# Performance work log

Hardware: AMD Instinct MI355X
Metric: run time of the kernel (lower is better)

The kernel has to match this reference:

```python
import jax, jax.numpy as jnp
import numpy as np

B, T, C = 2, 2048, 1024
H, HS = 16, 64
THETA = 10000.0


def _rope_tables(seq_len, dim, dtype):
    inv_freq = 1.0 / (THETA ** (jnp.arange(0, dim, 2, dtype=jnp.float32) / dim))
    t = jnp.arange(seq_len, dtype=jnp.float32)
    freqs = t[:, None] * inv_freq[None, :]          # [T, dim/2]
    emb = jnp.concatenate([freqs, freqs], axis=-1)  # [T, dim]
    return jnp.cos(emb).astype(dtype), jnp.sin(emb).astype(dtype)


def _rotate_half(x):
    x1, x2 = jnp.split(x, 2, axis=-1)
    return jnp.concatenate([-x2, x1], axis=-1)


def setup_inputs() -> dict:
    key = jax.random.key(0)
    ks = jax.random.split(key, 9)
    s = 0.02
    return {
        "q_x": jax.random.normal(ks[0], (B, T, C), dtype=jnp.float32),
        "wq": jax.random.normal(ks[1], (C, H * HS), dtype=jnp.float32) * s,
        "bq": jnp.zeros((H * HS,), dtype=jnp.float32),
        "wk": jax.random.normal(ks[2], (C, H * HS), dtype=jnp.float32) * s,
        "bk": jnp.zeros((H * HS,), dtype=jnp.float32),
        "wv": jax.random.normal(ks[3], (C, H * HS), dtype=jnp.float32) * s,
        "bv": jnp.zeros((H * HS,), dtype=jnp.float32),
        "wc": jax.random.normal(ks[4], (H * HS, C), dtype=jnp.float32) * s,
        "bc": jnp.zeros((C,), dtype=jnp.float32),
    }


def reference(q_x, wq, bq, wk, bk, wv, bv, wc, bc):
    b, t, _ = q_x.shape
    # Q/K/V projections -> [B, H, T, HS]
    q = (q_x @ wq + bq).reshape(b, t, H, HS).transpose(0, 2, 1, 3)
    k = (q_x @ wk + bk).reshape(b, t, H, HS).transpose(0, 2, 1, 3)
    v = (q_x @ wv + bv).reshape(b, t, H, HS).transpose(0, 2, 1, 3)
    # RoPE (concat-half rotation)
    cos, sin = _rope_tables(t, HS, q.dtype)  # [T, HS]
    q = q * cos + _rotate_half(q) * sin
    k = k * cos + _rotate_half(k) * sin
    # Naive causal attention
    scale = 1.0 / np.sqrt(HS)
    att = jnp.einsum("bhqd,bhkd->bhqk", q, k) * scale
    mask = jnp.tril(jnp.ones((t, t), dtype=bool))
    att = jnp.where(mask, att, -jnp.inf)
    att = jax.nn.softmax(att, axis=-1)
    y = jnp.einsum("bhqk,bhkd->bhqd", att, v)
    y = y.transpose(0, 2, 1, 3).reshape(b, t, H * HS)
    return y @ wc + bc
```

## Files before the change

### kernel.cpp

```cpp
#include <hip/hip_runtime.h>

#define B_  2
#define T_  2048
#define C_  1024
#define H_  16
#define HS_ 64
#define M_  4096
#define N_  1024
#define K_  1024

typedef float floatx4 __attribute__((ext_vector_type(4)));
typedef short bf16x8  __attribute__((ext_vector_type(8)));

__device__ __forceinline__ float bf2f(unsigned short u) {
    return __uint_as_float(((unsigned int)u) << 16);
}
__device__ __forceinline__ unsigned short f2bf(float f) {
    unsigned int u = __float_as_uint(f);
    return (unsigned short)((u + 0x7fffu + ((u >> 16) & 1u)) >> 16);
}
__device__ __forceinline__ unsigned int pack2(float a, float b) {
    return (unsigned int)f2bf(a) | ((unsigned int)f2bf(b) << 16);
}
__device__ __forceinline__ unsigned int pack2t(float a, float b) {
    return __builtin_amdgcn_perm(__float_as_uint(b), __float_as_uint(a), 0x07060302u);
}
__device__ __forceinline__ void async16(const unsigned short* g, unsigned short* l) {
    __builtin_amdgcn_global_load_lds(
        (const __attribute__((address_space(1))) unsigned int*)g,
        (__attribute__((address_space(3))) unsigned int*)l, 16, 0, 0);
}

__global__ __launch_bounds__(256) void prep_kernel(
    const float* __restrict__ x,
    const float* __restrict__ w0, const float* __restrict__ w1,
    const float* __restrict__ w2, const float* __restrict__ w3,
    unsigned short* __restrict__ xb, unsigned short* __restrict__ wTall)
{
    __shared__ float tile[64][65];
    const int bid = blockIdx.x;
    const int t = threadIdx.x;
    if (bid < 4096) {
        const size_t i = ((size_t)bid * 256 + t) * 4;
        const float4 v = *(const float4*)(x + i);
        ushort4 st;
        st.x = f2bf(v.x); st.y = f2bf(v.y); st.z = f2bf(v.z); st.w = f2bf(v.w);
        *(ushort4*)(xb + i) = st;
        return;
    }
    const int zb = bid - 4096;
    const int z = zb >> 8, rem = zb & 255;
    const float* w = (z == 0) ? w0 : (z == 1) ? w1 : (z == 2) ? w2 : w3;
    unsigned short* wT = wTall + ((size_t)z << 20);
    const int n0 = (rem & 15) * 64, k0 = (rem >> 4) * 64;

    const int r = t >> 2, cq = (t & 3) * 16;
    const float4* src = (const float4*)(w + (size_t)(k0 + r) * N_ + n0 + cq);
    const float4 v0 = src[0], v1 = src[1], v2 = src[2], v3 = src[3];
    tile[r][cq+0]=v0.x; tile[r][cq+1]=v0.y; tile[r][cq+2]=v0.z; tile[r][cq+3]=v0.w;
    tile[r][cq+4]=v1.x; tile[r][cq+5]=v1.y; tile[r][cq+6]=v1.z; tile[r][cq+7]=v1.w;
    tile[r][cq+8]=v2.x; tile[r][cq+9]=v2.y; tile[r][cq+10]=v2.z; tile[r][cq+11]=v2.w;
    tile[r][cq+12]=v3.x; tile[r][cq+13]=v3.y; tile[r][cq+14]=v3.z; tile[r][cq+15]=v3.w;
    __syncthreads();

    const int rn = t >> 2, ck = (t & 3) * 16;
    unsigned int o[8];
#pragma unroll
    for (int ii = 0; ii < 8; ii++)
        o[ii] = pack2(tile[ck + 2*ii][rn], tile[ck + 2*ii + 1][rn]);
    unsigned short* dst = wT + (size_t)(n0 + rn) * K_ + k0 + ck;
    *(uint4*)dst       = make_uint4(o[0], o[1], o[2], o[3]);
    *(uint4*)(dst + 8) = make_uint4(o[4], o[5], o[6], o[7]);
}

__global__ __launch_bounds__(512, 2) void qkv_gemm(
    const unsigned short* __restrict__ xb, const unsigned short* __restrict__ wT,
    const float* __restrict__ bq, const float* __restrict__ bk,
    const float* __restrict__ bv,
    unsigned short* __restrict__ qb, unsigned short* __restrict__ kb,
    unsigned short* __restrict__ vb)
{
    __shared__ unsigned short lds[65536];

    const int tid  = threadIdx.x;
    const int lane = tid & 63;
    const int wave = tid >> 6;

    const int bid = blockIdx.x;
    const int swz = (bid & 7) * 24 + (bid >> 3);
    const int nb  = swz % 12;
    const int mb  = swz / 12;
    const int m0  = mb * 256;
    const int n0g = nb * 256;

    const int wm = wave >> 2, wn = wave & 3;
    const int fr = lane & 15, quad = lane >> 4;

    const int r_s = tid >> 2;
    const int c_s = (tid & 3) ^ ((tid >> 3) & 3);
    const unsigned short* aS0 = xb + (size_t)(m0 + r_s) * 1024 + c_s * 8;
    const unsigned short* aS1 = aS0 + (size_t)128 * 1024;
    const unsigned short* bS0 = wT + (size_t)(n0g + r_s) * 1024 + c_s * 8;
    const unsigned short* bS1 = bS0 + (size_t)128 * 1024;
    unsigned short* ldw = &lds[wave * 512];

    auto stage = [&](int buf, int region, const unsigned short* s0,
                     const unsigned short* s1) {
        unsigned short* d = ldw + buf * 32768 + region * 8192;
        async16(s0, d);
        async16(s1, d + 4096);
    };

    int oA[8], oB[4];
#pragma unroll
    for (int i = 0; i < 8; i++) {
        const int r = wm * 128 + i * 16 + fr;
        oA[i] = r * 32 + ((quad ^ ((r >> 1) & 3)) << 3);
    }
#pragma unroll
    for (int j = 0; j < 4; j++) {
        const int r = wn * 64 + j * 16 + fr;
        oB[j] = r * 32 + ((quad ^ ((r >> 1) & 3)) << 3);
    }

    floatx4 acc[8][4];
#pragma unroll
    for (int i = 0; i < 8; i++)
#pragma unroll
        for (int j = 0; j < 4; j++) acc[i][j] = (floatx4){0.f, 0.f, 0.f, 0.f};

    stage(0, 0, aS0,      aS1);
    stage(0, 2, bS0,      bS1);
    stage(0, 1, aS0 + 32, aS1 + 32);
    stage(0, 3, bS0 + 32, bS1 + 32);
    stage(1, 0, aS0 + 64, aS1 + 64);
    stage(1, 2, bS0 + 64, bS1 + 64);
    asm volatile("s_waitcnt vmcnt(8)" ::: "memory");
    __builtin_amdgcn_s_barrier();
    __builtin_amdgcn_sched_barrier(0);

    bf16x8 af[4], bfr[4];
#pragma unroll 2
    for (int t = 0; t < 16; ++t) {
        const int cur = t & 1, nxt = cur ^ 1;
        const unsigned short* A0 = &lds[cur * 32768];
        const unsigned short* A1 = A0 + 8192;
        const unsigned short* B0 = A0 + 16384;
        const unsigned short* B1 = A0 + 24576;
        const int k1 = (t + 1) * 64, k2 = (t + 2) * 64;

#pragma unroll
        for (int i = 0; i < 4; i++) af[i]  = *(const bf16x8*)&A0[oA[i]];
#pragma unroll
        for (int j = 0; j < 4; j++) bfr[j] = *(const bf16x8*)&B0[oB[j]];
        if (t + 1 < 16) stage(nxt, 1, aS0 + k1 + 32, aS1 + k1 + 32);
        __builtin_amdgcn_s_barrier();
        asm volatile("s_waitcnt lgkmcnt(0)" ::: "memory");
        __builtin_amdgcn_s_setprio(1);
#pragma unroll
        for (int i = 0; i < 4; i++)
#pragma unroll
            for (int j = 0; j < 4; j++)
                acc[i][j] = __builtin_amdgcn_mfma_f32_16x16x32_bf16(
                    af[i], bfr[j], acc[i][j], 0, 0, 0);
        __builtin_amdgcn_s_setprio(0);
        __builtin_amdgcn_s_barrier();
        __builtin_amdgcn_sched_barrier(0);

#pragma unroll
        for (int i = 0; i < 4; i++) af[i] = *(const bf16x8*)&A0[oA[4 + i]];
        if (t + 1 < 16) stage(nxt, 3, bS0 + k1 + 32, bS1 + k1 + 32);
        asm volatile("s_waitcnt vmcnt(8)" ::: "memory");
        __builtin_amdgcn_s_barrier();
        asm volatile("s_waitcnt lgkmcnt(0)" ::: "memory");
        __builtin_amdgcn_s_setprio(1);
#pragma unroll
        for (int i = 0; i < 4; i++)
#pragma unroll
            for (int j = 0; j < 4; j++)
                acc[4 + i][j] = __builtin_amdgcn_mfma_f32_16x16x32_bf16(
                    af[i], bfr[j], acc[4 + i][j], 0, 0, 0);
        __builtin_amdgcn_s_setprio(0);
        __builtin_amdgcn_s_barrier();
        __builtin_amdgcn_sched_barrier(0);

#pragma unroll
        for (int i = 0; i < 4; i++) af[i]  = *(const bf16x8*)&A1[oA[i]];
#pragma unroll
        for (int j = 0; j < 4; j++) bfr[j] = *(const bf16x8*)&B1[oB[j]];
        if (t + 2 < 16) stage(cur, 0, aS0 + k2, aS1 + k2);
        __builtin_amdgcn_s_barrier();
        asm volatile("s_waitcnt lgkmcnt(0)" ::: "memory");
        __builtin_amdgcn_s_setprio(1);
#pragma unroll
        for (int i = 0; i < 4; i++)
#pragma unroll
            for (int j = 0; j < 4; j++)
                acc[i][j] = __builtin_amdgcn_mfma_f32_16x16x32_bf16(
                    af[i], bfr[j], acc[i][j], 0, 0, 0);
        __builtin_amdgcn_s_setprio(0);
        __builtin_amdgcn_s_barrier();
        __builtin_amdgcn_sched_barrier(0);

#pragma unroll
        for (int i = 0; i < 4; i++) af[i] = *(const bf16x8*)&A1[oA[4 + i]];
        if (t + 2 < 16) stage(cur, 2, bS0 + k2, bS1 + k2);
        asm volatile("s_waitcnt vmcnt(8)" ::: "memory");
        __builtin_amdgcn_s_barrier();
        asm volatile("s_waitcnt lgkmcnt(0)" ::: "memory");
        __builtin_amdgcn_s_setprio(1);
#pragma unroll
        for (int i = 0; i < 4; i++)
#pragma unroll
            for (int j = 0; j < 4; j++)
                acc[4 + i][j] = __builtin_amdgcn_mfma_f32_16x16x32_bf16(
                    af[i], bfr[j], acc[4 + i][j], 0, 0, 0);
        __builtin_amdgcn_s_setprio(0);
        __builtin_amdgcn_s_barrier();
        __builtin_amdgcn_sched_barrier(0);
    }

    const int p = nb >> 2;
    const int colbase = (nb & 3) * 256 + wn * 64;
    const int h = colbase >> 6;
    const int rb = quad * 4;
    const float* bias = (p == 0) ? bq : (p == 1) ? bk : bv;

    if (p == 2) {
#pragma unroll
        for (int j = 0; j < 4; j++) {
            const int d = j * 16 + fr;
            const float bz = bias[colbase + d];
#pragma unroll
            for (int i = 0; i < 8; i++) {
                const int row0 = m0 + wm * 128 + i * 16 + rb;
                const int bb = row0 >> 11, tt = row0 & 2047;
                ushort4 st;
                st.x = f2bf(acc[i][j][0] + bz);
                st.y = f2bf(acc[i][j][1] + bz);
                st.z = f2bf(acc[i][j][2] + bz);
                st.w = f2bf(acc[i][j][3] + bz);
                *(ushort4*)&vb[((size_t)(bb * H_ + h) * HS_ + d) * T_ + tt] = st;
            }
        }
    } else {
        unsigned short* out = (p == 0) ? qb : kb;
        const float qsc = (p == 0) ? 0.18033688011111772f : 1.0f;
        const float bz0 = bias[colbase + fr];
        const float bz1 = bias[colbase + 16 + fr];
        const float bz2 = bias[colbase + 32 + fr];
        const float bz3 = bias[colbase + 48 + fr];
        const float nl = -0.41524101186279297f;
        const float if0 = exp2f((float)fr * nl);
        const float if1 = exp2f((float)(fr + 16) * nl);
#pragma unroll
        for (int i = 0; i < 8; i++) {
#pragma unroll
            for (int pr = 0; pr < 4; pr++) {
                const int row = m0 + wm * 128 + i * 16 + rb + pr;
                const int bb = row >> 11, tt = row & 2047;
                float s0, c0, s1, c1;
                __sincosf((float)tt * if0, &s0, &c0);
                __sincosf((float)tt * if1, &s1, &c1);
                const float v0 = acc[i][0][pr] + bz0;
                const float v1 = acc[i][1][pr] + bz1;
                const float v2 = acc[i][2][pr] + bz2;
                const float v3 = acc[i][3][pr] + bz3;
                unsigned short* ob = out + ((size_t)(bb * H_ + h) * T_ + tt) * HS_ + fr;
                ob[0]  = f2bf((v0 * c0 - v2 * s0) * qsc);
                ob[16] = f2bf((v1 * c1 - v3 * s1) * qsc);
                ob[32] = f2bf((v2 * c0 + v0 * s0) * qsc);
                ob[48] = f2bf((v3 * c1 + v1 * s1) * qsc);
            }
        }
    }
}

__global__ __launch_bounds__(256) void attn_kernel(
    const unsigned short* __restrict__ qb, const unsigned short* __restrict__ kb,
    const unsigned short* __restrict__ vt, unsigned short* __restrict__ yb,
    unsigned short* __restrict__ Opart, float* __restrict__ Mpart)
{
    __shared__ unsigned short Ks[2][64 * 64];
    __shared__ unsigned short Vs[2][64 * 64];
    __shared__ unsigned short Ps[4][16 * 64];

    const int bh = blockIdx.x;
    const int b = bh >> 4, h = bh & 15;
    const int s = 47 - (int)blockIdx.y;
    int qt, ktlo, kthi, half;
    bool split;
    if (s < 16) { qt = s; ktlo = 0; kthi = qt; half = 0; split = false; }
    else {
        const int idx = s - 16;
        qt = 16 + (idx >> 1); half = idx & 1;
        const int nf = (qt + 2) >> 1;
        ktlo = half ? nf : 0;
        kthi = half ? qt : nf - 1;
        split = true;
    }
    const int r0 = qt * 64;
    const int tid  = threadIdx.x;
    const int lane = tid & 63;
    const int wave = tid >> 6;
    const int l4   = lane & 15;
    const int quad = lane >> 4;

    const int qrow_g = r0 + wave * 16 + l4;

    bf16x8 qf[2];
    {
        const unsigned short* qp = qb + ((size_t)bh * T_ + qrow_g) * HS_ + quad * 8;
        qf[0] = *(const bf16x8*)(qp);
        qf[1] = *(const bf16x8*)(qp + 32);
    }

    floatx4 o[4];
#pragma unroll
    for (int g = 0; g < 4; g++) o[g] = (floatx4){0.f, 0.f, 0.f, 0.f};
    float m = -1e30f, l = 0.f;

    const int srow = tid >> 2;
    const int sc16 = (tid & 3) * 16;
    const int ssw  = (srow & 7) * 8;
    const int psw  = (l4 & 7) * 8;

    const unsigned short* kp = kb + ((size_t)bh * T_ + srow) * HS_ + sc16;
    const unsigned short* vp = vt + ((size_t)(bh * 64 + srow)) * T_ + sc16;

    uint4 rk0 = *(const uint4*)(kp + (size_t)ktlo * 64 * HS_);
    uint4 rk1 = *(const uint4*)(kp + (size_t)ktlo * 64 * HS_ + 8);
    uint4 rv0 = *(const uint4*)(vp + ktlo * 64);
    uint4 rv1 = *(const uint4*)(vp + ktlo * 64 + 8);
    *(uint4*)&Ks[0][srow * 64 + ( sc16      ^ ssw)] = rk0;
    *(uint4*)&Ks[0][srow * 64 + ((sc16 + 8) ^ ssw)] = rk1;
    *(uint4*)&Vs[0][srow * 64 + ( sc16      ^ ssw)] = rv0;
    *(uint4*)&Vs[0][srow * 64 + ((sc16 + 8) ^ ssw)] = rv1;

    for (int kt = ktlo; kt <= kthi; kt++) {
        const int cur = (kt - ktlo) & 1;
        if (kt < kthi) {
            const unsigned short* kpn = kp + (size_t)(kt + 1) * (64 * HS_);
            const unsigned short* vpn = vp + (kt + 1) * 64;
            rk0 = *(const uint4*)kpn;
            rk1 = *(const uint4*)(kpn + 8);
            rv0 = *(const uint4*)vpn;
            rv1 = *(const uint4*)(vpn + 8);
        }
        __syncthreads();

        floatx4 sf[4];
#pragma unroll
        for (int mg = 0; mg < 4; mg++) {
            const int key = mg * 16 + l4;
            const int ksw = (key & 7) * 8;
            const bf16x8 a0 = *(const bf16x8*)&Ks[cur][key * 64 + ( (quad * 8)       ^ ksw)];
            const bf16x8 a1 = *(const bf16x8*)&Ks[cur][key * 64 + (((quad * 8) + 32) ^ ksw)];
            floatx4 z = (floatx4){0.f, 0.f, 0.f, 0.f};
            z = __builtin_amdgcn_mfma_f32_16x16x32_bf16(a0, qf[0], z, 0, 0, 0);
            z = __builtin_amdgcn_mfma_f32_16x16x32_bf16(a1, qf[1], z, 0, 0, 0);
            sf[mg] = z;
        }

        if (kt == qt) {
#pragma unroll
            for (int mg = 0; mg < 4; mg++)
#pragma unroll
                for (int r = 0; r < 4; r++)
                    if (kt * 64 + 16 * mg + quad * 4 + r > qrow_g)
                        sf[mg][r] = -1e30f;
        }

        float tm = sf[0][0];
#pragma unroll
        for (int mg = 0; mg < 4; mg++)
#pragma unroll
            for (int r = 0; r < 4; r++) tm = fmaxf(tm, sf[mg][r]);
        tm = fmaxf(tm, __shfl_xor(tm, 16));
        tm = fmaxf(tm, __shfl_xor(tm, 32));
        const float mnew  = fmaxf(m, tm);
        const float alpha = __builtin_amdgcn_exp2f(m - mnew);

        float p[4][4];
        float ps = 0.f;
#pragma unroll
        for (int mg = 0; mg < 4; mg++)
#pragma unroll
            for (int r = 0; r < 4; r++) {
                p[mg][r] = __builtin_amdgcn_exp2f(sf[mg][r] - mnew);
                ps += p[mg][r];
            }
        ps += __shfl_xor(ps, 16);
        ps += __shfl_xor(ps, 32);
        l = l * alpha + ps;
        m = mnew;
#pragma unroll
        for (int g = 0; g < 4; g++) o[g] = o[g] * alpha;

#pragma unroll
        for (int mg = 0; mg < 4; mg++) {
            const int kb4 = 16 * mg + quad * 4;
            const int off = ((kb4 & ~7) ^ psw) | (kb4 & 7);
            uint2 w;
            w.x = pack2t(p[mg][0], p[mg][1]);
            w.y = pack2t(p[mg][2], p[mg][3]);
            *(uint2*)&Ps[wave][l4 * 64 + off] = w;
        }

        const bf16x8 pf0 = *(const bf16x8*)&Ps[wave][l4 * 64 + ( (quad * 8)       ^ psw)];
        const bf16x8 pf1 = *(const bf16x8*)&Ps[wave][l4 * 64 + (((quad * 8) + 32) ^ psw)];
#pragma unroll
        for (int g = 0; g < 4; g++) {
            const int vd  = g * 16 + l4;
            const int vsw = (vd & 7) * 8;
            const bf16x8 va0 = *(const bf16x8*)&Vs[cur][vd * 64 + ( (quad * 8)       ^ vsw)];
            const bf16x8 va1 = *(const bf16x8*)&Vs[cur][vd * 64 + (((quad * 8) + 32) ^ vsw)];
            o[g] = __builtin_amdgcn_mfma_f32_16x16x32_bf16(va0, pf0, o[g], 0, 0, 0);
            o[g] = __builtin_amdgcn_mfma_f32_16x16x32_bf16(va1, pf1, o[g], 0, 0, 0);
        }

        if (kt < kthi) {
            const int nxt = cur ^ 1;
            *(uint4*)&Ks[nxt][srow * 64 + ( sc16      ^ ssw)] = rk0;
            *(uint4*)&Ks[nxt][srow * 64 + ((sc16 + 8) ^ ssw)] = rk1;
            *(uint4*)&Vs[nxt][srow * 64 + ( sc16      ^ ssw)] = rv0;
            *(uint4*)&Vs[nxt][srow * 64 + ((sc16 + 8) ^ ssw)] = rv1;
        }
    }

    if (!split) {
        const float invl = 1.f / l;
        unsigned short* yrow = yb + ((size_t)(b * T_ + qrow_g) * H_ + h) * HS_;
#pragma unroll
        for (int g = 0; g < 4; g++) {
            ushort4 st;
            st.x = f2bf(o[g][0] * invl);
            st.y = f2bf(o[g][1] * invl);
            st.z = f2bf(o[g][2] * invl);
            st.w = f2bf(o[g][3] * invl);
            *(ushort4*)&yrow[16 * g + quad * 4] = st;
        }
    } else {
        const int u  = (bh * 16 + (qt - 16)) * 2 + half;
        const int rl = wave * 16 + l4;
        unsigned short* Op = Opart + (size_t)u * 4096 + rl * 64;
#pragma unroll
        for (int g = 0; g < 4; g++) {
            ushort4 st;
            st.x = f2bf(o[g][0]);
            st.y = f2bf(o[g][1]);
            st.z = f2bf(o[g][2]);
            st.w = f2bf(o[g][3]);
            *(ushort4*)&Op[16 * g + quad * 4] = st;
        }
        if (quad == 0) {
            float* ml = Mpart + (size_t)u * 128;
            ml[rl]      = m;
            ml[64 + rl] = l;
        }
    }
}

__global__ __launch_bounds__(256) void attn_combine(
    const unsigned short* __restrict__ Opart, const float* __restrict__ Mpart,
    unsigned short* __restrict__ yb)
{
    const int u  = blockIdx.x;
    const int bh = u >> 4, qt = 16 + (u & 15);
    const int b = bh >> 4, h = bh & 15;
    const int t = threadIdx.x;
    const int r = t >> 2, c = (t & 3) * 16;

    const float* ml1 = Mpart + (size_t)(u * 2) * 128;
    const float* ml2 = ml1 + 128;
    const float m1 = ml1[r], l1 = ml1[64 + r];
    const float m2 = ml2[r], l2 = ml2[64 + r];
    const float M  = fmaxf(m1, m2);
    const float w1 = __builtin_amdgcn_exp2f(m1 - M);
    const float w2 = __builtin_amdgcn_exp2f(m2 - M);
    const float inv = 1.f / (l1 * w1 + l2 * w2);
    const float a1 = w1 * inv, a2 = w2 * inv;

    const unsigned short* O1 = Opart + (size_t)(u * 2)     * 4096 + r * 64 + c;
    const unsigned short* O2 = Opart + (size_t)(u * 2 + 1) * 4096 + r * 64 + c;
    unsigned short* yrow = yb + ((size_t)(b * T_ + qt * 64 + r) * H_ + h) * HS_ + c;

#pragma unroll
    for (int j = 0; j < 2; j++) {
        const uint4 u1 = *(const uint4*)(O1 + 8 * j);
        const uint4 u2 = *(const uint4*)(O2 + 8 * j);
        const unsigned int a[4] = {u1.x, u1.y, u1.z, u1.w};
        const unsigned int d[4] = {u2.x, u2.y, u2.z, u2.w};
        unsigned int ov[4];
#pragma unroll
        for (int q = 0; q < 4; q++) {
            const float y0 = bf2f((unsigned short)(a[q] & 0xffff)) * a1
                           + bf2f((unsigned short)(d[q] & 0xffff)) * a2;
            const float y1 = bf2f((unsigned short)(a[q] >> 16)) * a1
                           + bf2f((unsigned short)(d[q] >> 16)) * a2;
            ov[q] = pack2(y0, y1);
        }
        *(uint4*)(yrow + 8 * j) = make_uint4(ov[0], ov[1], ov[2], ov[3]);
    }
}

__global__ __launch_bounds__(256) void out_gemm(
    const unsigned short* __restrict__ A, const unsigned short* __restrict__ wcT,
    const float* __restrict__ bias, float* __restrict__ out)
{
    __shared__ unsigned short As[2 * 64 * 32];
    __shared__ unsigned short Bs[2 * 128 * 32];

    const int tid  = threadIdx.x;
    const int lane = tid & 63;
    const int wave = tid >> 6;
    const int n0 = blockIdx.x * 128;
    const int m0 = blockIdx.y * 64;

    const int lrow = lane >> 2, lch = (lane & 3) * 8;
    const unsigned short* ag  = A   + (size_t)(m0 + wave * 16 + lrow) * K_ + lch;
    const unsigned short* bg0 = wcT + (size_t)(n0 + wave * 32 + lrow) * K_ + lch;
    const unsigned short* bg1 = bg0 + (size_t)16 * K_;
    unsigned short* lA0  = &As[(wave * 16) * 32];
    unsigned short* lA1  = lA0 + 2048;
    unsigned short* lB00 = &Bs[(wave * 32) * 32];
    unsigned short* lB01 = &Bs[(wave * 32 + 16) * 32];
    unsigned short* lB10 = lB00 + 4096;
    unsigned short* lB11 = lB01 + 4096;

    const int fr = lane & 15;
    const int fk = (lane >> 4) * 8;
    const int wr2 = wave >> 1, wc2 = wave & 1;

    floatx4 acc[2][4];
#pragma unroll
    for (int i = 0; i < 2; i++)
#pragma unroll
        for (int j = 0; j < 4; j++) acc[i][j] = (floatx4){0.f, 0.f, 0.f, 0.f};

    for (int k0 = 0; k0 < K_; k0 += 64) {
        __syncthreads();
        async16(ag  + k0,      lA0);
        async16(ag  + k0 + 32, lA1);
        async16(bg0 + k0,      lB00);
        async16(bg1 + k0,      lB01);
        async16(bg0 + k0 + 32, lB10);
        async16(bg1 + k0 + 32, lB11);
        __syncthreads();

#pragma unroll
        for (int kh = 0; kh < 2; kh++) {
            const unsigned short* Ah = &As[kh * 2048];
            const unsigned short* Bh = &Bs[kh * 4096];
            bf16x8 af[2], bfr[4];
#pragma unroll
            for (int i = 0; i < 2; i++)
                af[i] = *(const bf16x8*)&Ah[(wr2 * 32 + i * 16 + fr) * 32 + fk];
#pragma unroll
            for (int j = 0; j < 4; j++)
                bfr[j] = *(const bf16x8*)&Bh[(wc2 * 64 + j * 16 + fr) * 32 + fk];
#pragma unroll
            for (int i = 0; i < 2; i++)
#pragma unroll
                for (int j = 0; j < 4; j++)
                    acc[i][j] = __builtin_amdgcn_mfma_f32_16x16x32_bf16(
                        af[i], bfr[j], acc[i][j], 0, 0, 0);
        }
    }

    const int rbase = (lane >> 4) * 4;
#pragma unroll
    for (int j = 0; j < 4; j++) {
        const int col = n0 + wc2 * 64 + j * 16 + fr;
        const float bz = bias[col];
#pragma unroll
        for (int i = 0; i < 2; i++) {
#pragma unroll
            for (int pr = 0; pr < 4; pr++) {
                const int row = m0 + wr2 * 32 + i * 16 + rbase + pr;
                out[(size_t)row * N_ + col] = acc[i][j][pr] + bz;
            }
        }
    }
}

extern "C" void kernel_launch(void* const* d_in, const int* in_sizes, int n_in,
                              void* d_out, int out_size, void* d_ws, size_t ws_size,
                              hipStream_t stream) {
    const float* x  = (const float*)d_in[0];
    const float* wq = (const float*)d_in[1];
    const float* bq = (const float*)d_in[2];
    const float* wk = (const float*)d_in[3];
    const float* bk = (const float*)d_in[4];
    const float* wv = (const float*)d_in[5];
    const float* bv = (const float*)d_in[6];
    const float* wc = (const float*)d_in[7];
    const float* bc = (const float*)d_in[8];
    float* out = (float*)d_out;

    unsigned short* ws  = (unsigned short*)d_ws;
    unsigned short* qb  = ws;
    unsigned short* kb  = ws + (size_t)4194304;
    unsigned short* vb  = ws + (size_t)8388608;
    unsigned short* yb  = ws + (size_t)12582912;
    unsigned short* xb  = ws + (size_t)16777216;
    unsigned short* wT  = ws + (size_t)20971520;
    unsigned short* wcT = wT + ((size_t)3 << 20);
    unsigned short* Opart = xb;
    float*          Mpart = (float*)wT;

    prep_kernel<<<5120, 256, 0, stream>>>(x, wq, wk, wv, wc, xb, wT);
    qkv_gemm<<<192, 512, 0, stream>>>(xb, wT, bq, bk, bv, qb, kb, vb);
    attn_kernel<<<dim3(32, 48), 256, 0, stream>>>(qb, kb, vb, yb, Opart, Mpart);
    attn_combine<<<512, 256, 0, stream>>>(Opart, Mpart, yb);
    out_gemm<<<dim3(8, 64), 256, 0, stream>>>(yb, wcT, bc, out);
}
```

Before: 188.1 us.

## Single-buffer K/V LDS, lazy softmax rescale, MFMA priority hints in attention

Replaces the double-buffered K/V shared tiles with a single buffer, written at the top of each iteration between two barriers, while the next tile is still prefetched into registers. Adds a lazy online-softmax rescale that skips the alpha correction unless some row max rises more than 8 (log2 units) above the running max. Wraps the MFMA loops in s_setprio hints and rebalances the max and sum reductions into trees. This halves K/V LDS use, which may allow more blocks per CU, and cuts exp and multiply work, but adds a barrier per iteration and lets p values reach up to 2^8 before bf16 packing.

```diff
diff --git a/kernel.cpp b/kernel.cpp
--- a/kernel.cpp
+++ b/kernel.cpp
@@ -281,8 +281,8 @@
     const unsigned short* __restrict__ vt, unsigned short* __restrict__ yb,
     unsigned short* __restrict__ Opart, float* __restrict__ Mpart)
 {
-    __shared__ unsigned short Ks[2][64 * 64];
-    __shared__ unsigned short Vs[2][64 * 64];
+    __shared__ unsigned short Ks[64 * 64];
+    __shared__ unsigned short Vs[64 * 64];
     __shared__ unsigned short Ps[4][16 * 64];
 
     const int bh = blockIdx.x;
@@ -332,13 +332,13 @@
     uint4 rk1 = *(const uint4*)(kp + (size_t)ktlo * 64 * HS_ + 8);
     uint4 rv0 = *(const uint4*)(vp + ktlo * 64);
     uint4 rv1 = *(const uint4*)(vp + ktlo * 64 + 8);
-    *(uint4*)&Ks[0][srow * 64 + ( sc16      ^ ssw)] = rk0;
-    *(uint4*)&Ks[0][srow * 64 + ((sc16 + 8) ^ ssw)] = rk1;
-    *(uint4*)&Vs[0][srow * 64 + ( sc16      ^ ssw)] = rv0;
-    *(uint4*)&Vs[0][srow * 64 + ((sc16 + 8) ^ ssw)] = rv1;
 
     for (int kt = ktlo; kt <= kthi; kt++) {
-        const int cur = (kt - ktlo) & 1;
+        __syncthreads();
+        *(uint4*)&Ks[srow * 64 + ( sc16      ^ ssw)] = rk0;
+        *(uint4*)&Ks[srow * 64 + ((sc16 + 8) ^ ssw)] = rk1;
+        *(uint4*)&Vs[srow * 64 + ( sc16      ^ ssw)] = rv0;
+        *(uint4*)&Vs[srow * 64 + ((sc16 + 8) ^ ssw)] = rv1;
         if (kt < kthi) {
             const unsigned short* kpn = kp + (size_t)(kt + 1) * (64 * HS_);
             const unsigned short* vpn = vp + (kt + 1) * 64;
@@ -350,17 +350,19 @@
         __syncthreads();
 
         floatx4 sf[4];
+        __builtin_amdgcn_s_setprio(1);
 #pragma unroll
         for (int mg = 0; mg < 4; mg++) {
             const int key = mg * 16 + l4;
             const int ksw = (key & 7) * 8;
-            const bf16x8 a0 = *(const bf16x8*)&Ks[cur][key * 64 + ( (quad * 8)       ^ ksw)];
-            const bf16x8 a1 = *(const bf16x8*)&Ks[cur][key * 64 + (((quad * 8) + 32) ^ ksw)];
+            const bf16x8 a0 = *(const bf16x8*)&Ks[key * 64 + ( (quad * 8)       ^ ksw)];
+            const bf16x8 a1 = *(const bf16x8*)&Ks[key * 64 + (((quad * 8) + 32) ^ ksw)];
             floatx4 z = (floatx4){0.f, 0.f, 0.f, 0.f};
             z = __builtin_amdgcn_mfma_f32_16x16x32_bf16(a0, qf[0], z, 0, 0, 0);
             z = __builtin_amdgcn_mfma_f32_16x16x32_bf16(a1, qf[1], z, 0, 0, 0);
             sf[mg] = z;
         }
+        __builtin_amdgcn_s_setprio(0);
 
         if (kt == qt) {
 #pragma unroll
@@ -371,31 +373,37 @@
                         sf[mg][r] = -1e30f;
         }
 
-        float tm = sf[0][0];
+        float mx[4];
 #pragma unroll
         for (int mg = 0; mg < 4; mg++)
-#pragma unroll
-            for (int r = 0; r < 4; r++) tm = fmaxf(tm, sf[mg][r]);
+            mx[mg] = fmaxf(fmaxf(sf[mg][0], sf[mg][1]),
+                           fmaxf(sf[mg][2], sf[mg][3]));
+        float tm = fmaxf(fmaxf(mx[0], mx[1]), fmaxf(mx[2], mx[3]));
         tm = fmaxf(tm, __shfl_xor(tm, 16));
         tm = fmaxf(tm, __shfl_xor(tm, 32));
-        const float mnew  = fmaxf(m, tm);
-        const float alpha = __builtin_amdgcn_exp2f(m - mnew);
+
+        if (!__all(tm <= m + 8.f)) {
+            const float mnew  = fmaxf(m, tm);
+            const float alpha = __builtin_amdgcn_exp2f(m - mnew);
+            l *= alpha;
+#pragma unroll
+            for (int g = 0; g < 4; g++) o[g] = o[g] * alpha;
+            m = mnew;
+        }
 
         float p[4][4];
-        float ps = 0.f;
-#pragma unroll
-        for (int mg = 0; mg < 4; mg++)
-#pragma unroll
-            for (int r = 0; r < 4; r++) {
-                p[mg][r] = __builtin_amdgcn_exp2f(sf[mg][r] - mnew);
-                ps += p[mg][r];
-            }
+        float psg[4];
+#pragma unroll
+        for (int mg = 0; mg < 4; mg++) {
+#pragma unroll
+            for (int r = 0; r < 4; r++)
+                p[mg][r] = __builtin_amdgcn_exp2f(sf[mg][r] - m);
+            psg[mg] = (p[mg][0] + p[mg][1]) + (p[mg][2] + p[mg][3]);
+        }
+        float ps = (psg[0] + psg[1]) + (psg[2] + psg[3]);
         ps += __shfl_xor(ps, 16);
         ps += __shfl_xor(ps, 32);
-        l = l * alpha + ps;
-        m = mnew;
-#pragma unroll
-        for (int g = 0; g < 4; g++) o[g] = o[g] * alpha;
+        l += ps;
 
 #pragma unroll
         for (int mg = 0; mg < 4; mg++) {
@@ -409,23 +417,17 @@
 
         const bf16x8 pf0 = *(const bf16x8*)&Ps[wave][l4 * 64 + ( (quad * 8)       ^ psw)];
         const bf16x8 pf1 = *(const bf16x8*)&Ps[wave][l4 * 64 + (((quad * 8) + 32) ^ psw)];
+        __builtin_amdgcn_s_setprio(1);
 #pragma unroll
         for (int g = 0; g < 4; g++) {
             const int vd  = g * 16 + l4;
             const int vsw = (vd & 7) * 8;
-            const bf16x8 va0 = *(const bf16x8*)&Vs[cur][vd * 64 + ( (quad * 8)       ^ vsw)];
-            const bf16x8 va1 = *(const bf16x8*)&Vs[cur][vd * 64 + (((quad * 8) + 32) ^ vsw)];
+            const bf16x8 va0 = *(const bf16x8*)&Vs[vd * 64 + ( (quad * 8)       ^ vsw)];
+            const bf16x8 va1 = *(const bf16x8*)&Vs[vd * 64 + (((quad * 8) + 32) ^ vsw)];
             o[g] = __builtin_amdgcn_mfma_f32_16x16x32_bf16(va0, pf0, o[g], 0, 0, 0);
             o[g] = __builtin_amdgcn_mfma_f32_16x16x32_bf16(va1, pf1, o[g], 0, 0, 0);
         }
-
-        if (kt < kthi) {
-            const int nxt = cur ^ 1;
-            *(uint4*)&Ks[nxt][srow * 64 + ( sc16      ^ ssw)] = rk0;
-            *(uint4*)&Ks[nxt][srow * 64 + ((sc16 + 8) ^ ssw)] = rk1;
-            *(uint4*)&Vs[nxt][srow * 64 + ( sc16      ^ ssw)] = rv0;
-            *(uint4*)&Vs[nxt][srow * 64 + ((sc16 + 8) ^ ssw)] = rv1;
-        }
+        __builtin_amdgcn_s_setprio(0);
     }
 
     if (!split) {
```

Result: no change. 189.7 us (+0.9%).

## Lazily rescale online softmax, defer row-sum reduction, raise MFMA wave priority

Applied to the files above, without the earlier changes.

The attention inner loop now skips the running-max update and the rescaling of the accumulator whenever no lane's tile maximum exceeds the current max by more than 8 (log2 domain). It also keeps the row sum of probabilities per lane and reduces it across lanes once after the loop, instead of two cross-lane shuffles per tile. Both matrix-core blocks are wrapped in s_setprio so waves issuing MFMA get scheduling priority. The skip lets unnormalised probabilities reach up to 256 before conversion to bf16 and adds a wave-wide vote on every tile.

```diff
diff --git a/kernel.cpp b/kernel.cpp
--- a/kernel.cpp
+++ b/kernel.cpp
@@ -350,6 +350,7 @@
         __syncthreads();
 
         floatx4 sf[4];
+        __builtin_amdgcn_s_setprio(1);
 #pragma unroll
         for (int mg = 0; mg < 4; mg++) {
             const int key = mg * 16 + l4;
@@ -361,6 +362,7 @@
             z = __builtin_amdgcn_mfma_f32_16x16x32_bf16(a1, qf[1], z, 0, 0, 0);
             sf[mg] = z;
         }
+        __builtin_amdgcn_s_setprio(0);
 
         if (kt == qt) {
 #pragma unroll
@@ -371,31 +373,34 @@
                         sf[mg][r] = -1e30f;
         }
 
-        float tm = sf[0][0];
+        float mx[4];
 #pragma unroll
         for (int mg = 0; mg < 4; mg++)
-#pragma unroll
-            for (int r = 0; r < 4; r++) tm = fmaxf(tm, sf[mg][r]);
-        tm = fmaxf(tm, __shfl_xor(tm, 16));
-        tm = fmaxf(tm, __shfl_xor(tm, 32));
-        const float mnew  = fmaxf(m, tm);
-        const float alpha = __builtin_amdgcn_exp2f(m - mnew);
+            mx[mg] = fmaxf(fmaxf(sf[mg][0], sf[mg][1]),
+                           fmaxf(sf[mg][2], sf[mg][3]));
+        float tm = fmaxf(fmaxf(mx[0], mx[1]), fmaxf(mx[2], mx[3]));
+
+        if (!__all(tm <= m + 8.f)) {
+            tm = fmaxf(tm, __shfl_xor(tm, 16));
+            tm = fmaxf(tm, __shfl_xor(tm, 32));
+            const float mnew  = fmaxf(m, tm);
+            const float alpha = __builtin_amdgcn_exp2f(m - mnew);
+            l *= alpha;
+#pragma unroll
+            for (int g = 0; g < 4; g++) o[g] = o[g] * alpha;
+            m = mnew;
+        }
 
         float p[4][4];
-        float ps = 0.f;
-#pragma unroll
-        for (int mg = 0; mg < 4; mg++)
-#pragma unroll
-            for (int r = 0; r < 4; r++) {
-                p[mg][r] = __builtin_amdgcn_exp2f(sf[mg][r] - mnew);
-                ps += p[mg][r];
-            }
-        ps += __shfl_xor(ps, 16);
-        ps += __shfl_xor(ps, 32);
-        l = l * alpha + ps;
-        m = mnew;
-#pragma unroll
-        for (int g = 0; g < 4; g++) o[g] = o[g] * alpha;
+        float psg[4];
+#pragma unroll
+        for (int mg = 0; mg < 4; mg++) {
+#pragma unroll
+            for (int r = 0; r < 4; r++)
+                p[mg][r] = __builtin_amdgcn_exp2f(sf[mg][r] - m);
+            psg[mg] = (p[mg][0] + p[mg][1]) + (p[mg][2] + p[mg][3]);
+        }
+        l += (psg[0] + psg[1]) + (psg[2] + psg[3]);
 
 #pragma unroll
         for (int mg = 0; mg < 4; mg++) {
@@ -409,6 +414,7 @@
 
         const bf16x8 pf0 = *(const bf16x8*)&Ps[wave][l4 * 64 + ( (quad * 8)       ^ psw)];
         const bf16x8 pf1 = *(const bf16x8*)&Ps[wave][l4 * 64 + (((quad * 8) + 32) ^ psw)];
+        __builtin_amdgcn_s_setprio(1);
 #pragma unroll
         for (int g = 0; g < 4; g++) {
             const int vd  = g * 16 + l4;
@@ -418,6 +424,7 @@
             o[g] = __builtin_amdgcn_mfma_f32_16x16x32_bf16(va0, pf0, o[g], 0, 0, 0);
             o[g] = __builtin_amdgcn_mfma_f32_16x16x32_bf16(va1, pf1, o[g], 0, 0, 0);
         }
+        __builtin_amdgcn_s_setprio(0);
 
         if (kt < kthi) {
             const int nxt = cur ^ 1;
@@ -427,6 +434,9 @@
             *(uint4*)&Vs[nxt][srow * 64 + ((sc16 + 8) ^ ssw)] = rv1;
         }
     }
+
+    l += __shfl_xor(l, 16);
+    l += __shfl_xor(l, 32);
 
     if (!split) {
         const float invl = 1.f / l;
```

Result: no change. 188.6 us (+0.3%).
